# Optimization experiments

Hardware: AMD Instinct MI355X
Metric: run time of the kernel (lower is better)

## Reference

```python
import jax, jax.numpy as jnp
import numpy as np

Q_DIM = 512
K_DIM = 512
HID = 512


def setup_inputs() -> dict:
    key = jax.random.key(0)
    k1, k2, k3, k4, k5, k6 = jax.random.split(key, 6)
    b, n_q, s = 4, 64, 1024
    queries = jax.random.normal(k1, (b, n_q, Q_DIM), dtype=jnp.float32)
    keys = jax.random.normal(k2, (b, s, K_DIM), dtype=jnp.float32)
    values = jax.random.normal(k3, (b, s, 512), dtype=jnp.float32)
    lim1 = 1.0 / np.sqrt(Q_DIM + K_DIM)
    W1 = jax.random.uniform(k4, (HID, Q_DIM + K_DIM), minval=-lim1, maxval=lim1, dtype=jnp.float32)
    b1 = jax.random.uniform(k5, (HID,), minval=-lim1, maxval=lim1, dtype=jnp.float32)
    lim2 = 1.0 / np.sqrt(HID)
    w2 = jax.random.uniform(k6, (HID,), minval=-lim2, maxval=lim2, dtype=jnp.float32)
    return {"queries": queries, "keys": keys, "values": values,
            "W1": W1, "b1": b1, "w2": w2}


def reference(queries, keys, values, W1, b1, w2):
    # linear1 on concat([q, k]) == W1q @ q + W1k @ k (split the weight),
    # avoiding materializing the concatenated [b, n_q, s, q_v+k_v] tensor.
    W1q = W1[:, :Q_DIM]  # [hid, q_dim]
    W1k = W1[:, Q_DIM:]  # [hid, k_dim]
    q_proj = jnp.einsum('bqd,hd->bqh', queries, W1q)          # [b, n_q, hid]
    k_proj = jnp.einsum('bsd,hd->bsh', keys, W1k) + b1        # [b, s, hid]
    hidden = jnp.tanh(q_proj[:, :, None, :] + k_proj[:, None, :, :])  # [b, n_q, s, hid]
    scores = jnp.einsum('bqsh,h->bqs', hidden, w2)            # [b, n_q, s]
    attn = jax.nn.softmax(scores, axis=2)                     # softmax over key axis
    final = jnp.einsum('bqs,bsv->bqv', attn, values)          # [b, n_q, v_dim]
    return final
```

## Files before the change

kernel.cpp:

```cpp
#include <hip/hip_runtime.h>


static constexpr int SLEN = 1024;
static constexpr int DIM  = 512;
static constexpr float TANH_SCALE = 2.885390081777927f;

typedef __attribute__((ext_vector_type(8))) short bf16x8;
typedef __attribute__((ext_vector_type(4))) float f32x4;

__device__ __forceinline__ float fast_exp2(float x) { return __builtin_amdgcn_exp2f(x); }
__device__ __forceinline__ float fast_rcp(float x)  { return __builtin_amdgcn_rcpf(x); }

__device__ __forceinline__ unsigned int f2bf(float f) {
    unsigned int u = __float_as_uint(f);
    u += 0x7FFF + ((u >> 16) & 1);
    return u >> 16;
}

__device__ __forceinline__ void async_copy16(const void* g, void* l) {
    __builtin_amdgcn_global_load_lds(
        (const __attribute__((address_space(1))) unsigned int*)g,
        (__attribute__((address_space(3))) unsigned int*)l, 16, 0, 0);
}

__global__ __launch_bounds__(256) void convert_bf16(
    const float* __restrict__ q, const float* __restrict__ k,
    const float* __restrict__ w, unsigned short* __restrict__ qb,
    unsigned short* __restrict__ kb, unsigned short* __restrict__ wb)
{
    int id = blockIdx.x * 256 + threadIdx.x;
    const float* src; unsigned short* dst; int off;
    if (id < 32768)        { src = q; dst = qb; off = id; }
    else if (id < 557056)  { src = k; dst = kb; off = id - 32768; }
    else                   { src = w; dst = wb; off = id - 557056; }
    float4 v = ((const float4*)src)[off];
    ushort4 o;
    o.x = (unsigned short)f2bf(v.x); o.y = (unsigned short)f2bf(v.y);
    o.z = (unsigned short)f2bf(v.z); o.w = (unsigned short)f2bf(v.w);
    ((ushort4*)dst)[off] = o;
}

__global__ __launch_bounds__(256) void proj_mfma(
    const unsigned short* __restrict__ qb, const unsigned short* __restrict__ kb,
    const unsigned short* __restrict__ wb, const float* __restrict__ b1,
    float* __restrict__ qp, float* __restrict__ kp)
{
    __shared__ __align__(16) unsigned short As[64][64];
    __shared__ __align__(16) unsigned short Ws[64][64];

    const int bx = blockIdx.x;
    const unsigned short* A; float* C; const float* bias; int mb, nb, col_off;
    if (bx < 512) {
        A = kb; C = kp; bias = b1; col_off = 512;
        mb = (bx >> 3) * 64; nb = (bx & 7) * 64;
    } else {
        int b2 = bx - 512;
        A = qb; C = qp; bias = nullptr; col_off = 0;
        mb = (b2 >> 3) * 64; nb = (b2 & 7) * 64;
    }

    const int t = threadIdx.x;
    const int l = t & 63;
    const int wv = t >> 6;
    const int wm = (wv & 1) * 32;
    const int wn = (wv >> 1) * 32;
    const int lane16 = l & 15;
    const int quad   = l >> 4;
    const int r8   = l >> 3;
    const int schk = (l & 7) ^ r8;

    f32x4 acc[2][2] = {{{0.f,0.f,0.f,0.f},{0.f,0.f,0.f,0.f}},
                       {{0.f,0.f,0.f,0.f},{0.f,0.f,0.f,0.f}}};

    for (int kc = 0; kc < DIM; kc += 64) {
#pragma unroll
        for (int i = 0; i < 2; ++i) {
            int rbase = wv * 16 + i * 8;
            async_copy16(A + (size_t)(mb + rbase + r8) * DIM + kc + schk * 8, &As[rbase][0]);
            async_copy16(wb + (size_t)(nb + rbase + r8) * 1024 + col_off + kc + schk * 8, &Ws[rbase][0]);
        }
        __syncthreads();

#pragma unroll
        for (int ks = 0; ks < 2; ++ks) {
            int cc = ks * 4 + quad;
            int sw = (cc ^ (lane16 & 7)) << 3;
            bf16x8 a0  = *(const bf16x8*)&As[wm + lane16][sw];
            bf16x8 a1  = *(const bf16x8*)&As[wm + 16 + lane16][sw];
            bf16x8 b0  = *(const bf16x8*)&Ws[wn + lane16][sw];
            bf16x8 b1v = *(const bf16x8*)&Ws[wn + 16 + lane16][sw];
            acc[0][0] = __builtin_amdgcn_mfma_f32_16x16x32_bf16(a0, b0,  acc[0][0], 0, 0, 0);
            acc[0][1] = __builtin_amdgcn_mfma_f32_16x16x32_bf16(a0, b1v, acc[0][1], 0, 0, 0);
            acc[1][0] = __builtin_amdgcn_mfma_f32_16x16x32_bf16(a1, b0,  acc[1][0], 0, 0, 0);
            acc[1][1] = __builtin_amdgcn_mfma_f32_16x16x32_bf16(a1, b1v, acc[1][1], 0, 0, 0);
        }
        __syncthreads();
    }

#pragma unroll
    for (int mi = 0; mi < 2; ++mi) {
#pragma unroll
        for (int ni = 0; ni < 2; ++ni) {
            int col = nb + wn + 16 * ni + lane16;
            float bv = bias ? bias[col] : 0.0f;
#pragma unroll
            for (int r = 0; r < 4; ++r) {
                int row = mb + wm + 16 * mi + quad * 4 + r;
                C[(size_t)row * DIM + col] = fast_exp2((acc[mi][ni][r] + bv) * TANH_SCALE);
            }
        }
    }
}

__global__ __launch_bounds__(256) void scores_kernel(
    const float* __restrict__ qp, const float* __restrict__ kp,
    const float* __restrict__ w2, float* __restrict__ th)
{
    __shared__ __align__(16) float qs[16][68];
    __shared__ __align__(16) float ks[32][68];
    __shared__ __align__(16) float ws2[256];
    const int t     = threadIdx.x;
    const int sb    = blockIdx.x * 32;
    const int qt    = blockIdx.y & 3;
    const int half  = blockIdx.y >> 2;
    const int kbase = half * 256;
    const int qrow0 = blockIdx.z * 64 + qt * 16;
    const int krow0 = blockIdx.z * 1024 + sb;
    float* thh = th + (size_t)half * 256 * SLEN;

    if (t < 64) *(float4*)&ws2[t << 2] = *(const float4*)(w2 + kbase + (t << 2));

    const int tq = t >> 4;
    const int ts = t & 15;
    float a00 = 0.f, a01 = 0.f, a10 = 0.f, a11 = 0.f;

    for (int kc = 0; kc < 256; kc += 64) {
        {
            int r = t >> 4, g = (t & 15) << 2;
            *(float4*)&qs[r][g] = *(const float4*)(qp + (size_t)(qrow0 + r) * DIM + kbase + kc + g);
        }
#pragma unroll
        for (int rr = 0; rr < 2; ++rr) {
            int idx = t + rr * 256;
            int r = idx >> 4, g = (idx & 15) << 2;
            *(float4*)&ks[r][g] = *(const float4*)(kp + (size_t)(krow0 + r) * DIM + kbase + kc + g);
        }
        __syncthreads();
#pragma unroll
        for (int k4 = 0; k4 < 16; ++k4) {
            float4 qv = *(const float4*)&qs[tq][k4 << 2];
            float4 k0 = *(const float4*)&ks[ts][k4 << 2];
            float4 k1 = *(const float4*)&ks[ts + 16][k4 << 2];
            float4 wv = *(const float4*)&ws2[kc + (k4 << 2)];
            {
                float d0 = fmaf(qv.x, k0.x, 1.0f);
                float d1 = fmaf(qv.y, k0.y, 1.0f);
                a00 = fmaf(fmaf(wv.x, d1, wv.y * d0), fast_rcp(d0 * d1), a00);
                float d2 = fmaf(qv.z, k0.z, 1.0f);
                float d3 = fmaf(qv.w, k0.w, 1.0f);
                a01 = fmaf(fmaf(wv.z, d3, wv.w * d2), fast_rcp(d2 * d3), a01);
            }
            {
                float d0 = fmaf(qv.x, k1.x, 1.0f);
                float d1 = fmaf(qv.y, k1.y, 1.0f);
                a10 = fmaf(fmaf(wv.x, d1, wv.y * d0), fast_rcp(d0 * d1), a10);
                float d2 = fmaf(qv.z, k1.z, 1.0f);
                float d3 = fmaf(qv.w, k1.w, 1.0f);
                a11 = fmaf(fmaf(wv.z, d3, wv.w * d2), fast_rcp(d2 * d3), a11);
            }
        }
        __syncthreads();
    }
    thh[(size_t)(qrow0 + tq) * SLEN + sb + ts]      = -TANH_SCALE * (a00 + a01);
    thh[(size_t)(qrow0 + tq) * SLEN + sb + ts + 16] = -TANH_SCALE * (a10 + a11);
}

__global__ __launch_bounds__(256) void av_gemm(
    const float* __restrict__ th, const float* __restrict__ values,
    float* __restrict__ pt, float* __restrict__ sums_p)
{
    __shared__ __align__(16) float As[32][68];
    __shared__ __align__(16) float Bs[32][68];
    const int t  = threadIdx.x;
    const int nb = blockIdx.x * 64;
    const int kt = blockIdx.y;
    const int kb = kt * 128;
    const int b  = blockIdx.z;
    const int tx = t & 15, ty = t >> 4;
    float acc[4][4] = {};
    float rsum[2] = {0.f, 0.f};
    for (int kc = 0; kc < 128; kc += 32) {
        const int k0 = kb + kc;
#pragma unroll
        for (int r = 0; r < 2; ++r) {
            int idx = t + r * 256;
            int m   = idx >> 3;
            int k4  = (idx & 7) << 2;
            size_t base = (size_t)(b * 64 + m) * SLEN + k0 + k4;
            float4 t0 = *(const float4*)(th + base);
            float4 t1 = *(const float4*)(th + 262144 + base);
            float4 e;
            e.x = fast_exp2(t0.x + t1.x);
            e.y = fast_exp2(t0.y + t1.y);
            e.z = fast_exp2(t0.z + t1.z);
            e.w = fast_exp2(t0.w + t1.w);
            As[k4 + 0][m] = e.x; As[k4 + 1][m] = e.y;
            As[k4 + 2][m] = e.z; As[k4 + 3][m] = e.w;
            rsum[r] += e.x + e.y + e.z + e.w;
            int kk = idx >> 4;
            int g  = (idx & 15) << 2;
            *(float4*)&Bs[kk][g] =
                *(const float4*)(values + (size_t)(b * 1024 + k0 + kk) * DIM + nb + g);
        }
        __syncthreads();
#pragma unroll
        for (int k = 0; k < 32; ++k) {
            float4 a  = *(const float4*)&As[k][ty << 2];
            float4 bv = *(const float4*)&Bs[k][tx << 2];
            float am[4] = {a.x, a.y, a.z, a.w};
            float bn[4] = {bv.x, bv.y, bv.z, bv.w};
#pragma unroll
            for (int i = 0; i < 4; ++i)
#pragma unroll
                for (int j = 0; j < 4; ++j)
                    acc[i][j] = fmaf(am[i], bn[j], acc[i][j]);
        }
        __syncthreads();
    }
#pragma unroll
    for (int i = 0; i < 4; ++i) {
        int row = b * 64 + (ty << 2) + i;
        float4 o;
        o.x = acc[i][0]; o.y = acc[i][1]; o.z = acc[i][2]; o.w = acc[i][3];
        *(float4*)(pt + ((size_t)kt * 256 + row) * DIM + nb + (tx << 2)) = o;
    }
    if (nb == 0) {
#pragma unroll
        for (int r = 0; r < 2; ++r) {
            float v = rsum[r];
            v += __shfl_xor(v, 1, 64);
            v += __shfl_xor(v, 2, 64);
            v += __shfl_xor(v, 4, 64);
            if ((t & 7) == 0) {
                int m = (t >> 3) + r * 32;
                sums_p[kt * 256 + b * 64 + m] = v;
            }
        }
    }
}

__global__ __launch_bounds__(256) void reduce_kernel(
    const float* __restrict__ pt, const float* __restrict__ sums_p,
    float* __restrict__ out)
{
    int idx = blockIdx.x * 256 + threadIdx.x;
    const float4* p = (const float4*)pt;
    float4 a = p[idx];
#pragma unroll
    for (int k = 1; k < 8; ++k) {
        float4 v = p[k * 32768 + idx];
        a.x += v.x; a.y += v.y; a.z += v.z; a.w += v.w;
    }
    int row = idx >> 7;
    float s = 0.f;
#pragma unroll
    for (int k = 0; k < 8; ++k) s += sums_p[k * 256 + row];
    float r = fast_rcp(s);
    a.x *= r; a.y *= r; a.z *= r; a.w *= r;
    ((float4*)out)[idx] = a;
}

extern "C" void kernel_launch(void* const* d_in, const int* in_sizes, int n_in,
                              void* d_out, int out_size, void* d_ws, size_t ws_size,
                              hipStream_t stream) {
    const float* queries = (const float*)d_in[0];
    const float* keys    = (const float*)d_in[1];
    const float* values  = (const float*)d_in[2];
    const float* W1      = (const float*)d_in[3];
    const float* b1      = (const float*)d_in[4];
    const float* w2      = (const float*)d_in[5];
    float* out = (float*)d_out;

    float* qp     = (float*)d_ws;
    float* kp     = qp + 131072;
    float* th     = kp + 2097152;
    float* pt     = th + 2 * 262144;
    float* sums_p = pt + 8 * 131072;
    unsigned short* qbf = (unsigned short*)(sums_p + 2048);
    unsigned short* kbf = qbf + 131072;
    unsigned short* wbf = kbf + 2097152;
    (void)in_sizes; (void)n_in; (void)ws_size; (void)out_size;

    convert_bf16<<<dim3(2688), 256, 0, stream>>>(queries, keys, W1, qbf, kbf, wbf);
    proj_mfma<<<dim3(544), 256, 0, stream>>>(qbf, kbf, wbf, b1, qp, kp);
    scores_kernel<<<dim3(32, 8, 4), 256, 0, stream>>>(qp, kp, w2, th);
    av_gemm<<<dim3(8, 8, 4), 256, 0, stream>>>(th, values, pt, sums_p);
    reduce_kernel<<<dim3(128), 256, 0, stream>>>(pt, sums_p, out);
}
```

Measured before the change: 118.3 us.

## Fuse score computation with softmax-weighted value accumulation into one kernel

Merges the scores kernel and the attention-times-values GEMM: each block now covers the full hidden dimension, exponentiates its scores in LDS, and multiplies them by a 32-row slice of values to write partial outputs. This removes the intermediate score buffer round-trip and one launch. In exchange, the grid for the score phase halves, each block reloads values for all 512 output columns, the partial-output buffer grows from 8 to 32 splits, and the reduce kernel reads four times more partial data.

```diff
diff --git a/kernel.cpp b/kernel.cpp
--- a/kernel.cpp
+++ b/kernel.cpp
@@ -112,38 +112,41 @@
     }
 }
 
-__global__ __launch_bounds__(256) void scores_kernel(
+__global__ __launch_bounds__(256) void scores_av(
     const float* __restrict__ qp, const float* __restrict__ kp,
-    const float* __restrict__ w2, float* __restrict__ th)
+    const float* __restrict__ w2, const float* __restrict__ values,
+    float* __restrict__ pt, float* __restrict__ sums_p)
 {
     __shared__ __align__(16) float qs[16][68];
     __shared__ __align__(16) float ks[32][68];
-    __shared__ __align__(16) float ws2[256];
+    __shared__ __align__(16) float ws2[512];
+    __shared__ __align__(16) float es[16][33];
+    __shared__ __align__(16) float vs[32][68];
+
     const int t     = threadIdx.x;
-    const int sb    = blockIdx.x * 32;
-    const int qt    = blockIdx.y & 3;
-    const int half  = blockIdx.y >> 2;
-    const int kbase = half * 256;
-    const int qrow0 = blockIdx.z * 64 + qt * 16;
-    const int krow0 = blockIdx.z * 1024 + sb;
-    float* thh = th + (size_t)half * 256 * SLEN;
-
-    if (t < 64) *(float4*)&ws2[t << 2] = *(const float4*)(w2 + kbase + (t << 2));
+    const int st    = blockIdx.x;
+    const int sb    = st * 32;
+    const int qt    = blockIdx.y;
+    const int bb    = blockIdx.z;
+    const int qrow0 = bb * 64 + qt * 16;
+    const int krow0 = bb * 1024 + sb;
+
+    if (t < 128) *(float4*)&ws2[t << 2] = *(const float4*)(w2 + (t << 2));
 
     const int tq = t >> 4;
     const int ts = t & 15;
     float a00 = 0.f, a01 = 0.f, a10 = 0.f, a11 = 0.f;
 
-    for (int kc = 0; kc < 256; kc += 64) {
+    for (int kc = 0; kc < DIM; kc += 64) {
         {
             int r = t >> 4, g = (t & 15) << 2;
-            *(float4*)&qs[r][g] = *(const float4*)(qp + (size_t)(qrow0 + r) * DIM + kbase + kc + g);
+            *(float4*)&qs[r][g] = *(const float4*)(qp + (size_t)(qrow0 + r) * DIM + kc + g);
         }
 #pragma unroll
         for (int rr = 0; rr < 2; ++rr) {
             int idx = t + rr * 256;
             int r = idx >> 4, g = (idx & 15) << 2;
-            *(float4*)&ks[r][g] = *(const float4*)(kp + (size_t)(krow0 + r) * DIM + kbase + kc + g);
+            *(float4*)&ks[r][g] = *(const float4*)(kp + (size_t)(krow0 + r) * DIM + kc + g);
         }
         __syncthreads();
 #pragma unroll
@@ -171,80 +174,46 @@
         }
         __syncthreads();
     }
-    thh[(size_t)(qrow0 + tq) * SLEN + sb + ts]      = -TANH_SCALE * (a00 + a01);
-    thh[(size_t)(qrow0 + tq) * SLEN + sb + ts + 16] = -TANH_SCALE * (a10 + a11);
-}
-
-__global__ __launch_bounds__(256) void av_gemm(
-    const float* __restrict__ th, const float* __restrict__ values,
-    float* __restrict__ pt, float* __restrict__ sums_p)
-{
-    __shared__ __align__(16) float As[32][68];
-    __shared__ __align__(16) float Bs[32][68];
-    const int t  = threadIdx.x;
-    const int nb = blockIdx.x * 64;
-    const int kt = blockIdx.y;
-    const int kb = kt * 128;
-    const int b  = blockIdx.z;
-    const int tx = t & 15, ty = t >> 4;
-    float acc[4][4] = {};
-    float rsum[2] = {0.f, 0.f};
-    for (int kc = 0; kc < 128; kc += 32) {
-        const int k0 = kb + kc;
-#pragma unroll
-        for (int r = 0; r < 2; ++r) {
-            int idx = t + r * 256;
-            int m   = idx >> 3;
-            int k4  = (idx & 7) << 2;
-            size_t base = (size_t)(b * 64 + m) * SLEN + k0 + k4;
-            float4 t0 = *(const float4*)(th + base);
-            float4 t1 = *(const float4*)(th + 262144 + base);
-            float4 e;
-            e.x = fast_exp2(t0.x + t1.x);
-            e.y = fast_exp2(t0.y + t1.y);
-            e.z = fast_exp2(t0.z + t1.z);
-            e.w = fast_exp2(t0.w + t1.w);
-            As[k4 + 0][m] = e.x; As[k4 + 1][m] = e.y;
-            As[k4 + 2][m] = e.z; As[k4 + 3][m] = e.w;
-            rsum[r] += e.x + e.y + e.z + e.w;
-            int kk = idx >> 4;
-            int g  = (idx & 15) << 2;
-            *(float4*)&Bs[kk][g] =
-                *(const float4*)(values + (size_t)(b * 1024 + k0 + kk) * DIM + nb + g);
-        }
-        __syncthreads();
-#pragma unroll
-        for (int k = 0; k < 32; ++k) {
-            float4 a  = *(const float4*)&As[k][ty << 2];
-            float4 bv = *(const float4*)&Bs[k][tx << 2];
-            float am[4] = {a.x, a.y, a.z, a.w};
-            float bn[4] = {bv.x, bv.y, bv.z, bv.w};
-#pragma unroll
-            for (int i = 0; i < 4; ++i)
-#pragma unroll
-                for (int j = 0; j < 4; ++j)
-                    acc[i][j] = fmaf(am[i], bn[j], acc[i][j]);
-        }
-        __syncthreads();
-    }
-#pragma unroll
-    for (int i = 0; i < 4; ++i) {
-        int row = b * 64 + (ty << 2) + i;
-        float4 o;
-        o.x = acc[i][0]; o.y = acc[i][1]; o.z = acc[i][2]; o.w = acc[i][3];
-        *(float4*)(pt + ((size_t)kt * 256 + row) * DIM + nb + (tx << 2)) = o;
-    }
-    if (nb == 0) {
-#pragma unroll
-        for (int r = 0; r < 2; ++r) {
-            float v = rsum[r];
-            v += __shfl_xor(v, 1, 64);
-            v += __shfl_xor(v, 2, 64);
-            v += __shfl_xor(v, 4, 64);
-            if ((t & 7) == 0) {
-                int m = (t >> 3) + r * 32;
-                sums_p[kt * 256 + b * 64 + m] = v;
-            }
+
+    {
+        float e0 = fast_exp2(-TANH_SCALE * (a00 + a01));
+        float e1 = fast_exp2(-TANH_SCALE * (a10 + a11));
+        es[tq][ts]      = e0;
+        es[tq][ts + 16] = e1;
+        float v = e0 + e1;
+        v += __shfl_xor(v, 1, 64);
+        v += __shfl_xor(v, 2, 64);
+        v += __shfl_xor(v, 4, 64);
+        v += __shfl_xor(v, 8, 64);
+        if (ts == 0) sums_p[st * 256 + qrow0 + tq] = v;
+    }
+    __syncthreads();
+
+    {
+        const int q8 = t >> 4;
+        const int v4 = (t & 15) << 2;
+#pragma unroll
+        for (int vc = 0; vc < 8; ++vc) {
+#pragma unroll
+            for (int rr = 0; rr < 2; ++rr) {
+                int idx = t + rr * 256;
+                int r = idx >> 4, g = (idx & 15) << 2;
+                *(float4*)&vs[r][g] =
+                    *(const float4*)(values + (size_t)(krow0 + r) * DIM + vc * 64 + g);
+            }
+            __syncthreads();
+            float4 acc = {0.f, 0.f, 0.f, 0.f};
+#pragma unroll
+            for (int s = 0; s < 32; ++s) {
+                float ev = es[q8][s];
+                float4 vv = *(const float4*)&vs[s][v4];
+                acc.x = fmaf(ev, vv.x, acc.x);
+                acc.y = fmaf(ev, vv.y, acc.y);
+                acc.z = fmaf(ev, vv.z, acc.z);
+                acc.w = fmaf(ev, vv.w, acc.w);
+            }
+            *(float4*)(pt + ((size_t)st * 256 + qrow0 + q8) * DIM + vc * 64 + v4) = acc;
+            __syncthreads();
         }
     }
 }
@@ -257,14 +226,14 @@
     const float4* p = (const float4*)pt;
     float4 a = p[idx];
 #pragma unroll
-    for (int k = 1; k < 8; ++k) {
-        float4 v = p[k * 32768 + idx];
+    for (int k = 1; k < 32; ++k) {
+        float4 v = p[(size_t)k * 32768 + idx];
         a.x += v.x; a.y += v.y; a.z += v.z; a.w += v.w;
     }
     int row = idx >> 7;
     float s = 0.f;
 #pragma unroll
-    for (int k = 0; k < 8; ++k) s += sums_p[k * 256 + row];
+    for (int k = 0; k < 32; ++k) s += sums_p[k * 256 + row];
     float r = fast_rcp(s);
     a.x *= r; a.y *= r; a.z *= r; a.w *= r;
     ((float4*)out)[idx] = a;
@@ -283,17 +252,15 @@
 
     float* qp     = (float*)d_ws;
     float* kp     = qp + 131072;
-    float* th     = kp + 2097152;
-    float* pt     = th + 2 * 262144;
-    float* sums_p = pt + 8 * 131072;
-    unsigned short* qbf = (unsigned short*)(sums_p + 2048);
+    float* pt     = kp + 2097152;
+    float* sums_p = pt + 32 * 131072;
+    unsigned short* qbf = (unsigned short*)(sums_p + 8192);
     unsigned short* kbf = qbf + 131072;
     unsigned short* wbf = kbf + 2097152;
     (void)in_sizes; (void)n_in; (void)ws_size; (void)out_size;
 
     convert_bf16<<<dim3(2688), 256, 0, stream>>>(queries, keys, W1, qbf, kbf, wbf);
     proj_mfma<<<dim3(544), 256, 0, stream>>>(qbf, kbf, wbf, b1, qp, kp);
-    scores_kernel<<<dim3(32, 8, 4), 256, 0, stream>>>(qp, kp, w2, th);
-    av_gemm<<<dim3(8, 8, 4), 256, 0, stream>>>(th, values, pt, sums_p);
+    scores_av<<<dim3(32, 4, 4), 256, 0, stream>>>(qp, kp, w2, values, pt, sums_p);
     reduce_kernel<<<dim3(128), 256, 0, stream>>>(pt, sums_p, out);
 }
```

New measurement: 125.7 us. +6.2%, slower.
